# Kernel tuning notes

Measured on AMD Instinct MI355X. Metric: run time of the kernel, lower is better.

## Reference

```python
import jax, jax.numpy as jnp
import numpy as np

B, T, D_MODEL, HEAD = 4, 4096, 1024, 64

def setup_inputs() -> dict:
    key = jax.random.key(0)
    kq, kk, kv, kwq, kwk, kwv = jax.random.split(key, 6)
    q = jax.random.normal(kq, (B, T, D_MODEL), dtype=jnp.float32)
    k = jax.random.normal(kk, (B, T, D_MODEL), dtype=jnp.float32)
    v = jax.random.normal(kv, (B, T, D_MODEL), dtype=jnp.float32)
    # causal mask: mask==0 positions are filled with -inf before softmax
    mask = jnp.tril(jnp.ones((T, T), dtype=jnp.int32))
    s = 1.0 / np.sqrt(D_MODEL)
    Wq = jax.random.normal(kwq, (D_MODEL, HEAD), dtype=jnp.float32) * s
    Wk = jax.random.normal(kwk, (D_MODEL, HEAD), dtype=jnp.float32) * s
    Wv = jax.random.normal(kwv, (D_MODEL, HEAD), dtype=jnp.float32) * s
    return {"q": q, "k": k, "v": v, "Wq": Wq, "Wk": Wk, "Wv": Wv, "mask": mask}

def reference(q, k, v, Wq, Wk, Wv, mask):
    # projections: [B,T,D] @ [D,H] -> [B,T,H]
    qh = jnp.einsum('btd,dh->bth', q, Wq)
    kh = jnp.einsum('btd,dh->bth', k, Wk)
    vh = jnp.einsum('btd,dh->bth', v, Wv)
    scale = jnp.float32(HEAD) ** 0.5
    # full score matrix [B,T,T] (faithful to naive implementation)
    scores = jnp.einsum('bqh,bkh->bqk', qh, kh) / scale
    scores = jnp.where(mask == 0, -jnp.inf, scores)
    weights = jax.nn.softmax(scores, axis=-1)
    out = jnp.einsum('bqk,bkh->bqh', weights, vh)  # [B,T,H]
    return out
```

## Files before the change

### kernel.cpp

```cpp
#include <hip/hip_runtime.h>
#include <hip/hip_bf16.h>

#define BB 4
#define TT 4096
#define DM 1024
#define HH 64
#define RTOT (BB * TT)
#define SLOTS_PER_B 144
#define CHUNK 512

typedef __attribute__((ext_vector_type(4))) float f32x4;
typedef __attribute__((ext_vector_type(16))) float f32x16;
typedef __attribute__((ext_vector_type(8))) short s16x8;

#define EXP2(x) __builtin_amdgcn_exp2f(x)

__device__ __forceinline__ ushort f2bf_bits(float f) {
    union { float f; unsigned u; } x;
    x.f = f;
    unsigned r = x.u + 0x7FFFu + ((x.u >> 16) & 1u);
    return (ushort)(r >> 16);
}

__device__ __forceinline__ unsigned pack2bf(float lo, float hi) {
    return (unsigned)f2bf_bits(lo) | ((unsigned)f2bf_bits(hi) << 16);
}

__device__ __forceinline__ void gld_lds16(const void* g, void* l) {
    __builtin_amdgcn_global_load_lds(
        (const __attribute__((address_space(1))) void*)g,
        (__attribute__((address_space(3))) void*)l, 16, 0, 0);
}

__global__ __launch_bounds__(256) void k_wtrans(const float* __restrict__ wq,
                                                const float* __restrict__ wk,
                                                const float* __restrict__ wv,
                                                ushort* __restrict__ wt) {
    int idx = blockIdx.x * 256 + threadIdx.x;
    int m = idx >> 16, e = idx & 65535;
    int kk = e >> 11, r = e & 2047;
    int f = r >> 9, s = r & 511;
    int l = s >> 3, j = s & 7;
    int col = (l & 15) + 16 * f;
    int kd  = kk * 32 + (l >> 4) * 8 + j;
    const float* W = (m == 0) ? wq : (m == 1) ? wk : wv;
    float v = W[kd * HH + col];
    if (m == 0) v *= 0.1803368801111204f;
    wt[idx] = f2bf_bits(v);
}

__global__ __launch_bounds__(256) void k_proj(const float* __restrict__ q,
                                              const float* __restrict__ k,
                                              const float* __restrict__ v,
                                              const ushort* __restrict__ wt,
                                              ushort* __restrict__ qh,
                                              ushort* __restrict__ kh,
                                              ushort* __restrict__ vt) {
    int bid = blockIdx.x;
    int mat = bid >> 8;
    int rt  = bid & 255;
    const float* src = (mat == 0) ? q : (mat == 1) ? k : v;
    const ushort* w2 = wt + mat * 65536;

    __shared__ __align__(16) float abuf[4][3][512];

    int t = threadIdx.x;
    int wv_ = t >> 6, l = t & 63, lr = l & 15, lg = l >> 4;
    int rbase = rt * 64;
    int ph = bid & 31;

    int rowa = wv_ * 16 + (l >> 3);
    int ca   = (l & 7) ^ ((l >> 3) & 7);
    const float* ag0 = src + (size_t)(rbase + rowa) * DM + ca * 4;
    const float* ag1 = src + (size_t)(rbase + rowa + 8) * DM + ca * 4;

    int ax0 = (lr * 128 + lg * 32) ^ ((lr & 7) << 4);
    char* abase = (char*)&abuf[wv_][0][0];

    f32x4 acc[4] = {};
    s16x8 wA[4], wB[4];

#define KK(jj) (((jj) + ph) & 31)
#define LOADW(dst, jj) do { int kk_ = KK(jj);                                     \
    dst[0] = *reinterpret_cast<const s16x8*>(w2 + (kk_ * 4 + 0) * 512 + l * 8);   \
    dst[1] = *reinterpret_cast<const s16x8*>(w2 + (kk_ * 4 + 1) * 512 + l * 8);   \
    dst[2] = *reinterpret_cast<const s16x8*>(w2 + (kk_ * 4 + 2) * 512 + l * 8);   \
    dst[3] = *reinterpret_cast<const s16x8*>(w2 + (kk_ * 4 + 3) * 512 + l * 8); } while (0)
#define STAGEA(jj) do { int ko_ = KK(jj) * 32; int bo_ = ((jj) % 3) * 2048;       \
    gld_lds16(ag0 + ko_, abase + bo_);                                            \
    gld_lds16(ag1 + ko_, abase + bo_ + 1024); } while (0)

    LOADW(wA, 0);
    STAGEA(0);
    STAGEA(1);

#define BODY(jj, WCUR, WNXT) do {                                                 \
    if ((jj) + 1 < 32) LOADW(WNXT, (jj) + 1);                                     \
    if ((jj) + 2 < 32) STAGEA((jj) + 2);                                          \
    if ((jj) < 30)       asm volatile("s_waitcnt vmcnt(8)" ::: "memory");         \
    else if ((jj) == 30) asm volatile("s_waitcnt vmcnt(6)" ::: "memory");         \
    else                 asm volatile("s_waitcnt vmcnt(0)" ::: "memory");         \
    __builtin_amdgcn_sched_barrier(0);                                            \
    {                                                                             \
        const char* ab = abase + ((jj) % 3) * 2048;                               \
        f32x4 av0 = *reinterpret_cast<const f32x4*>(ab + ax0);                    \
        f32x4 av1 = *reinterpret_cast<const f32x4*>(ab + (ax0 ^ 16));             \
        s16x8 af;                                                                 \
        af[0] = f2bf_bits(av0[0]); af[1] = f2bf_bits(av0[1]);                     \
        af[2] = f2bf_bits(av0[2]); af[3] = f2bf_bits(av0[3]);                     \
        af[4] = f2bf_bits(av1[0]); af[5] = f2bf_bits(av1[1]);                     \
        af[6] = f2bf_bits(av1[2]); af[7] = f2bf_bits(av1[3]);                     \
        acc[0] = __builtin_amdgcn_mfma_f32_16x16x32_bf16(af, WCUR[0], acc[0], 0, 0, 0); \
        acc[1] = __builtin_amdgcn_mfma_f32_16x16x32_bf16(af, WCUR[1], acc[1], 0, 0, 0); \
        acc[2] = __builtin_amdgcn_mfma_f32_16x16x32_bf16(af, WCUR[2], acc[2], 0, 0, 0); \
        acc[3] = __builtin_amdgcn_mfma_f32_16x16x32_bf16(af, WCUR[3], acc[3], 0, 0, 0); \
    }                                                                             \
} while (0)

    for (int jj = 0; jj < 32; jj += 2) {
        BODY(jj, wA, wB);
        BODY(jj + 1, wB, wA);
    }
#undef BODY
#undef STAGEA
#undef LOADW
#undef KK

#pragma unroll
    for (int f = 0; f < 4; ++f)
#pragma unroll
        for (int r = 0; r < 4; ++r) {
            int row = rbase + wv_ * 16 + lg * 4 + r;
            int col = lr + 16 * f;
            ushort bv = f2bf_bits(acc[f][r]);
            if (mat == 0)      qh[row * HH + col] = bv;
            else if (mat == 1) kh[row * HH + col] = bv;
            else               vt[(size_t)col * RTOT + row] = bv;
        }
}

__global__ __launch_bounds__(256, 2) void k_attn(const ushort* __restrict__ qh,
                                                 const ushort* __restrict__ kh,
                                                 const ushort* __restrict__ vt,
                                                 float* __restrict__ pm,
                                                 float* __restrict__ pl,
                                                 float* __restrict__ pO) {
    int c = blockIdx.x, qt = blockIdx.y, b = blockIdx.z;
    int a = qt >> 2, r = qt & 3;
    int nch = a + 1;
    if (c >= nch) return;
    int slot = b * SLOTS_PER_B + 2 * a * (a + 1) + r * (a + 1) + c;

    __shared__ __align__(16) ushort kbuf[2][2048];
    __shared__ __align__(16) ushort vbuf[2][2048];

    int t = threadIdx.x, w = t >> 6, l = t & 63, lq = l & 31, hf = l >> 5;
    int W0 = qt * 128 + w * 32;
    size_t bT = (size_t)b * TT;
    int kv0 = c * CHUNK;
    int kvend = min(kv0 + CHUNK, (qt + 1) * 128);
    int nsteps = (kvend - kv0) >> 5;
    bool diag = (c == nch - 1);

    s16x8 qf[4];
#pragma unroll
    for (int s = 0; s < 4; ++s)
        qf[s] = *reinterpret_cast<const s16x8*>(qh + (bT + W0 + lq) * HH + s * 16 + hf * 8);

    int krow = t >> 3, kch = t & 7;
    int vrow = t >> 2, vch = t & 3;
    const ushort* kgp = kh + (bT + kv0 + krow) * HH + kch * 8;
    const ushort* vgp = vt + (size_t)vrow * RTOT + bT + kv0 + vch * 8;
    int kwo = (krow * 128 + kch * 16) ^ ((krow & 7) << 4);
    int vwo = (vrow * 64 + vch * 16) ^ ((vrow & 7) << 4);

    uint4 ks = *reinterpret_cast<const uint4*>(kgp);
    uint4 vs = *reinterpret_cast<const uint4*>(vgp);
    *reinterpret_cast<uint4*>(reinterpret_cast<char*>(&kbuf[0][0]) + kwo) = ks;
    *reinterpret_cast<uint4*>(reinterpret_cast<char*>(&vbuf[0][0]) + vwo) = vs;

    float m = -1e30f, ssum = 0.f;
    f32x16 oacc0 = {}, oacc1 = {};

    for (int j = 0; j < nsteps; ++j) {
        int cur = j & 1;
        if (j + 1 < nsteps) {
            ks = *reinterpret_cast<const uint4*>(kgp + (j + 1) * 32 * HH);
            vs = *reinterpret_cast<const uint4*>(vgp + (j + 1) * 32);
        }
        __syncthreads();
        int kvb = kv0 + j * 32;
        bool skip = diag && (kvb > W0 + 31);
        if (!skip) {
            const char* kb_ = reinterpret_cast<const char*>(&kbuf[cur][0]);
            const char* vb_ = reinterpret_cast<const char*>(&vbuf[cur][0]);
            f32x16 sacc = {};
#pragma unroll
            for (int s = 0; s < 4; ++s) {
                int ko = (lq * 128 + s * 32 + hf * 16) ^ ((lq & 7) << 4);
                s16x8 kf = *reinterpret_cast<const s16x8*>(kb_ + ko);
                sacc = __builtin_amdgcn_mfma_f32_32x32x16_bf16(kf, qf[s], sacc, 0, 0, 0);
            }
            if (diag && (kvb + 31 > W0)) {
                int qcol = W0 + lq;
#pragma unroll
                for (int g = 0; g < 16; ++g) {
                    int kvr = kvb + (g & 3) + 8 * (g >> 2) + 4 * hf;
                    if (kvr > qcol) sacc[g] = -1e30f;
                }
            }
            float t0 = fmaxf(fmaxf(fmaxf(sacc[0], sacc[1]), fmaxf(sacc[2], sacc[3])),
                             fmaxf(fmaxf(sacc[4], sacc[5]), fmaxf(sacc[6], sacc[7])));
            float t1 = fmaxf(fmaxf(fmaxf(sacc[8], sacc[9]), fmaxf(sacc[10], sacc[11])),
                             fmaxf(fmaxf(sacc[12], sacc[13]), fmaxf(sacc[14], sacc[15])));
            float tmx = fmaxf(t0, t1);
            tmx = fmaxf(tmx, __shfl_xor(tmx, 32));
            float mnew = fmaxf(m, tmx);
            float corr = EXP2(m - mnew);
            float p[16];
#pragma unroll
            for (int g = 0; g < 16; ++g) p[g] = EXP2(sacc[g] - mnew);
            float ts = ((p[0] + p[1]) + (p[2] + p[3])) + ((p[4] + p[5]) + (p[6] + p[7]))
                     + ((p[8] + p[9]) + (p[10] + p[11])) + ((p[12] + p[13]) + (p[14] + p[15]));
            ts += __shfl_xor(ts, 32);
            ssum = ssum * corr + ts;
            m = mnew;
#pragma unroll
            for (int g = 0; g < 16; ++g) { oacc0[g] *= corr; oacc1[g] *= corr; }
            unsigned d0 = pack2bf(p[0], p[1]),   d1 = pack2bf(p[2], p[3]);
            unsigned d2 = pack2bf(p[4], p[5]),   d3 = pack2bf(p[6], p[7]);
            unsigned d4 = pack2bf(p[8], p[9]),   d5 = pack2bf(p[10], p[11]);
            unsigned d6 = pack2bf(p[12], p[13]), d7 = pack2bf(p[14], p[15]);
            unsigned s0 = __shfl_xor(d0, 32), s1 = __shfl_xor(d1, 32);
            unsigned s2 = __shfl_xor(d2, 32), s3 = __shfl_xor(d3, 32);
            unsigned s4 = __shfl_xor(d4, 32), s5 = __shfl_xor(d5, 32);
            unsigned s6 = __shfl_xor(d6, 32), s7 = __shfl_xor(d7, 32);
            union { unsigned u[4]; s16x8 v; } pf0, pf1;
            pf0.u[0] = hf ? s2 : d0;  pf0.u[1] = hf ? s3 : d1;
            pf0.u[2] = hf ? d2 : s0;  pf0.u[3] = hf ? d3 : s1;
            pf1.u[0] = hf ? s6 : d4;  pf1.u[1] = hf ? s7 : d5;
            pf1.u[2] = hf ? d6 : s4;  pf1.u[3] = hf ? d7 : s5;
#pragma unroll
            for (int ts2 = 0; ts2 < 2; ++ts2) {
                int vo0 = ((0 * 32 + lq) * 64 + ts2 * 32 + hf * 16) ^ ((lq & 7) << 4);
                int vo1 = ((1 * 32 + lq) * 64 + ts2 * 32 + hf * 16) ^ ((lq & 7) << 4);
                s16x8 vf0 = *reinterpret_cast<const s16x8*>(vb_ + vo0);
                s16x8 vf1 = *reinterpret_cast<const s16x8*>(vb_ + vo1);
                s16x8 pf = ts2 ? pf1.v : pf0.v;
                oacc0 = __builtin_amdgcn_mfma_f32_32x32x16_bf16(vf0, pf, oacc0, 0, 0, 0);
                oacc1 = __builtin_amdgcn_mfma_f32_32x32x16_bf16(vf1, pf, oacc1, 0, 0, 0);
            }
        }
        __syncthreads();
        if (j + 1 < nsteps) {
            *reinterpret_cast<uint4*>(reinterpret_cast<char*>(&kbuf[cur ^ 1][0]) + kwo) = ks;
            *reinterpret_cast<uint4*>(reinterpret_cast<char*>(&vbuf[cur ^ 1][0]) + vwo) = vs;
        }
    }

    if (l < 32) {
        pm[(size_t)slot * 128 + w * 32 + l] = m;
        pl[(size_t)slot * 128 + w * 32 + l] = ssum;
    }
    float* po = pO + (size_t)slot * 8192;
#pragma unroll
    for (int g = 0; g < 16; ++g) {
        int hrow = (g & 3) + 8 * (g >> 2) + 4 * hf;
        po[hrow * 128 + w * 32 + lq] = oacc0[g];
        po[(32 + hrow) * 128 + w * 32 + lq] = oacc1[g];
    }
}

__global__ __launch_bounds__(256) void k_merge(const float* __restrict__ pm,
                                               const float* __restrict__ pl,
                                               const float* __restrict__ pO,
                                               float* __restrict__ out) {
    int qt = blockIdx.x & 31, b = blockIdx.x >> 5;
    int a = qt >> 2, r = qt & 3, nch = a + 1;
    int slot0 = b * SLOTS_PER_B + 2 * a * (a + 1) + r * (a + 1);

    __shared__ float wgt[8][128];
    __shared__ float invl[128];
    __shared__ float tr[64][130];

    int t = threadIdx.x;
    if (t < 128) {
        float M = -3e38f;
        for (int cc = 0; cc < nch; ++cc)
            M = fmaxf(M, pm[(size_t)(slot0 + cc) * 128 + t]);
        float L = 0.f;
        for (int cc = 0; cc < nch; ++cc) {
            float g = EXP2(pm[(size_t)(slot0 + cc) * 128 + t] - M);
            wgt[cc][t] = g;
            L += pl[(size_t)(slot0 + cc) * 128 + t] * g;
        }
        invl[t] = 1.0f / L;
    }
    __syncthreads();

    float4 acc[8] = {};
    for (int cc = 0; cc < nch; ++cc) {
        const float4* pp = reinterpret_cast<const float4*>(pO + (size_t)(slot0 + cc) * 8192);
#pragma unroll
        for (int it = 0; it < 8; ++it) {
            int idx = it * 256 + t, h = idx >> 5, qc = idx & 31;
            float4 vv = pp[h * 32 + qc];
            float4 w4 = *reinterpret_cast<const float4*>(&wgt[cc][qc * 4]);
            acc[it].x += vv.x * w4.x; acc[it].y += vv.y * w4.y;
            acc[it].z += vv.z * w4.z; acc[it].w += vv.w * w4.w;
        }
    }
#pragma unroll
    for (int it = 0; it < 8; ++it) {
        int idx = it * 256 + t, h = idx >> 5, qc = idx & 31;
        tr[h][qc * 4 + 0] = acc[it].x * invl[qc * 4 + 0];
        tr[h][qc * 4 + 1] = acc[it].y * invl[qc * 4 + 1];
        tr[h][qc * 4 + 2] = acc[it].z * invl[qc * 4 + 2];
        tr[h][qc * 4 + 3] = acc[it].w * invl[qc * 4 + 3];
    }
    __syncthreads();

    int q = t >> 1, half = t & 1;
    size_t obase = ((size_t)b * TT + qt * 128 + q) * 64 + half * 32;
#pragma unroll
    for (int jj = 0; jj < 8; ++jj) {
        float4 o;
        o.x = tr[half * 32 + jj * 4 + 0][q];
        o.y = tr[half * 32 + jj * 4 + 1][q];
        o.z = tr[half * 32 + jj * 4 + 2][q];
        o.w = tr[half * 32 + jj * 4 + 3][q];
        *reinterpret_cast<float4*>(out + obase + jj * 4) = o;
    }
}

extern "C" void kernel_launch(void* const* d_in, const int* in_sizes, int n_in,
                              void* d_out, int out_size, void* d_ws, size_t ws_size,
                              hipStream_t stream) {
    const float* q  = (const float*)d_in[0];
    const float* k  = (const float*)d_in[1];
    const float* v  = (const float*)d_in[2];
    const float* wq = (const float*)d_in[3];
    const float* wk = (const float*)d_in[4];
    const float* wv = (const float*)d_in[5];
    float* out = (float*)d_out;

    char* ws = (char*)d_ws;
    ushort* qh = (ushort*)(ws);
    ushort* kh = (ushort*)(ws + (2ull << 20));
    ushort* vt = (ushort*)(ws + (4ull << 20));
    ushort* wt = (ushort*)(ws + (6ull << 20));
    float*  pm = (float*)(ws + (7ull << 20));
    float*  pl = (float*)(ws + (7ull << 20) + (512u << 10));
    float*  pO = (float*)(ws + (8ull << 20));

    k_wtrans<<<768, 256, 0, stream>>>(wq, wk, wv, wt);
    k_proj<<<768, 256, 0, stream>>>(q, k, v, wt, qh, kh, vt);
    k_attn<<<dim3(8, 32, 4), 256, 0, stream>>>(qh, kh, vt, pm, pl, pO);
    k_merge<<<128, 256, 0, stream>>>(pm, pl, pO, out);
}
```

Measured before the change: 88.21 us.

## Split projection K dimension across two wave groups with LDS reduction

```diff
diff --git a/kernel.cpp b/kernel.cpp
--- a/kernel.cpp
+++ b/kernel.cpp
@@ -49,39 +49,40 @@
     wt[idx] = f2bf_bits(v);
 }
 
-__global__ __launch_bounds__(256) void k_proj(const float* __restrict__ q,
-                                              const float* __restrict__ k,
-                                              const float* __restrict__ v,
-                                              const ushort* __restrict__ wt,
-                                              ushort* __restrict__ qh,
-                                              ushort* __restrict__ kh,
-                                              ushort* __restrict__ vt) {
+__global__ __launch_bounds__(512, 6) void k_proj(const float* __restrict__ q,
+                                                 const float* __restrict__ k,
+                                                 const float* __restrict__ v,
+                                                 const ushort* __restrict__ wt,
+                                                 ushort* __restrict__ qh,
+                                                 ushort* __restrict__ kh,
+                                                 ushort* __restrict__ vt) {
     int bid = blockIdx.x;
     int mat = bid >> 8;
     int rt  = bid & 255;
     const float* src = (mat == 0) ? q : (mat == 1) ? k : v;
     const ushort* w2 = wt + mat * 65536;
 
-    __shared__ __align__(16) float abuf[4][3][512];
+    __shared__ __align__(16) char ldsx[49152];
 
     int t = threadIdx.x;
-    int wv_ = t >> 6, l = t & 63, lr = l & 15, lg = l >> 4;
+    int w = t >> 6, l = t & 63, lr = l & 15, lg = l >> 4;
+    int ws = w & 3, kh2 = w >> 2;
     int rbase = rt * 64;
-    int ph = bid & 31;
-
-    int rowa = wv_ * 16 + (l >> 3);
-    int ca   = (l & 7) ^ ((l >> 3) & 7);
-    const float* ag0 = src + (size_t)(rbase + rowa) * DM + ca * 4;
-    const float* ag1 = src + (size_t)(rbase + rowa + 8) * DM + ca * 4;
+    int ph = bid & 15;
+
+    int ca = (l & 7) ^ ((l >> 3) & 7);
+    const float* ag0 = src + (size_t)(rbase + ws * 16 + (l >> 3)) * DM + kh2 * 512 + ca * 4;
+    const float* ag1 = ag0 + 8 * DM;
+    char* abase = ldsx + w * 6144;
 
     int ax0 = (lr * 128 + lg * 32) ^ ((lr & 7) << 4);
-    char* abase = (char*)&abuf[wv_][0][0];
+    int wko = kh2 * 16;
 
     f32x4 acc[4] = {};
     s16x8 wA[4], wB[4];
 
-#define KK(jj) (((jj) + ph) & 31)
-#define LOADW(dst, jj) do { int kk_ = KK(jj);                                     \
+#define KK(jj) ((((jj) + ph) & 15))
+#define LOADW(dst, jj) do { int kk_ = wko + KK(jj);                               \
     dst[0] = *reinterpret_cast<const s16x8*>(w2 + (kk_ * 4 + 0) * 512 + l * 8);   \
     dst[1] = *reinterpret_cast<const s16x8*>(w2 + (kk_ * 4 + 1) * 512 + l * 8);   \
     dst[2] = *reinterpret_cast<const s16x8*>(w2 + (kk_ * 4 + 2) * 512 + l * 8);   \
@@ -90,16 +91,11 @@
     gld_lds16(ag0 + ko_, abase + bo_);                                            \
     gld_lds16(ag1 + ko_, abase + bo_ + 1024); } while (0)
 
-    LOADW(wA, 0);
-    STAGEA(0);
-    STAGEA(1);
-
-#define BODY(jj, WCUR, WNXT) do {                                                 \
-    if ((jj) + 1 < 32) LOADW(WNXT, (jj) + 1);                                     \
-    if ((jj) + 2 < 32) STAGEA((jj) + 2);                                          \
-    if ((jj) < 30)       asm volatile("s_waitcnt vmcnt(8)" ::: "memory");         \
-    else if ((jj) == 30) asm volatile("s_waitcnt vmcnt(6)" ::: "memory");         \
-    else                 asm volatile("s_waitcnt vmcnt(0)" ::: "memory");         \
+    LOADW(wA, 0); STAGEA(0);
+    LOADW(wB, 1); STAGEA(1);
+
+#define BODY(jj, WCUR, VM) do {                                                   \
+    asm volatile("s_waitcnt vmcnt(" #VM ")" ::: "memory");                        \
     __builtin_amdgcn_sched_barrier(0);                                            \
     {                                                                             \
         const char* ab = abase + ((jj) % 3) * 2048;                               \
@@ -115,28 +111,43 @@
         acc[2] = __builtin_amdgcn_mfma_f32_16x16x32_bf16(af, WCUR[2], acc[2], 0, 0, 0); \
         acc[3] = __builtin_amdgcn_mfma_f32_16x16x32_bf16(af, WCUR[3], acc[3], 0, 0, 0); \
     }                                                                             \
+    __builtin_amdgcn_sched_barrier(0);                                            \
+    if ((jj) + 2 < 16) { LOADW(WCUR, (jj) + 2); STAGEA((jj) + 2); }               \
 } while (0)
 
-    for (int jj = 0; jj < 32; jj += 2) {
-        BODY(jj, wA, wB);
-        BODY(jj + 1, wB, wA);
-    }
+    BODY(0,  wA, 6);  BODY(1,  wB, 6);  BODY(2,  wA, 6);  BODY(3,  wB, 6);
+    BODY(4,  wA, 6);  BODY(5,  wB, 6);  BODY(6,  wA, 6);  BODY(7,  wB, 6);
+    BODY(8,  wA, 6);  BODY(9,  wB, 6);  BODY(10, wA, 6);  BODY(11, wB, 6);
+    BODY(12, wA, 6);  BODY(13, wB, 6);  BODY(14, wA, 6);  BODY(15, wB, 0);
 #undef BODY
 #undef STAGEA
 #undef LOADW
 #undef KK
 
-#pragma unroll
-    for (int f = 0; f < 4; ++f)
-#pragma unroll
-        for (int r = 0; r < 4; ++r) {
-            int row = rbase + wv_ * 16 + lg * 4 + r;
-            int col = lr + 16 * f;
-            ushort bv = f2bf_bits(acc[f][r]);
-            if (mat == 0)      qh[row * HH + col] = bv;
-            else if (mat == 1) kh[row * HH + col] = bv;
-            else               vt[(size_t)col * RTOT + row] = bv;
-        }
+    __syncthreads();
+    float* xb = (float*)ldsx;
+    if (kh2 == 1) {
+#pragma unroll
+        for (int f = 0; f < 4; ++f)
+#pragma unroll
+            for (int r = 0; r < 4; ++r)
+                xb[ws * 1040 + (lg * 4 + r) * 65 + lr + 16 * f] = acc[f][r];
+    }
+    __syncthreads();
+    if (kh2 == 0) {
+#pragma unroll
+        for (int f = 0; f < 4; ++f)
+#pragma unroll
+            for (int r = 0; r < 4; ++r) {
+                float sum = acc[f][r] + xb[ws * 1040 + (lg * 4 + r) * 65 + lr + 16 * f];
+                int row = rbase + ws * 16 + lg * 4 + r;
+                int col = lr + 16 * f;
+                ushort bv = f2bf_bits(sum);
+                if (mat == 0)      qh[row * HH + col] = bv;
+                else if (mat == 1) kh[row * HH + col] = bv;
+                else               vt[(size_t)col * RTOT + row] = bv;
+            }
+    }
 }
 
 __global__ __launch_bounds__(256, 2) void k_attn(const ushort* __restrict__ qh,
@@ -354,7 +365,7 @@
     float*  pO = (float*)(ws + (8ull << 20));
 
     k_wtrans<<<768, 256, 0, stream>>>(wq, wk, wv, wt);
-    k_proj<<<768, 256, 0, stream>>>(q, k, v, wt, qh, kh, vt);
+    k_proj<<<768, 512, 0, stream>>>(q, k, v, wt, qh, kh, vt);
     k_attn<<<dim3(8, 32, 4), 256, 0, stream>>>(qh, kh, vt, pm, pl, pO);
     k_merge<<<128, 256, 0, stream>>>(pm, pl, pO, out);
 }
```

After: 87.84 us. No clear change (-0.4%).
